# Optimization experiments

Hardware: AMD Instinct MI355X
Metric: run time of the kernel (lower is better)

The kernel has to match this reference:

```python
import jax, jax.numpy as jnp
import numpy as np

DIM = 768
HEADS = 12
HEAD_DIM = DIM // HEADS
HIDDEN = int(DIM * 1.0)  # mlp_ratio = 1.0
EPS = 1e-5


def layer_norm(x, g, b):
    mu = jnp.mean(x, axis=-1, keepdims=True)
    var = jnp.mean(jnp.square(x - mu), axis=-1, keepdims=True)
    return (x - mu) * jax.lax.rsqrt(var + EPS) * g + b


def setup_inputs() -> dict:
    key = jax.random.key(0)
    ks = jax.random.split(key, 8)
    s = 0.02
    return {
        "x": jax.random.normal(ks[0], (8, 1024, DIM), dtype=jnp.float32),
        "mask": jnp.ones((8, 1024), dtype=jnp.int32),
        "g1": jnp.ones((DIM,), jnp.float32),
        "b1": jnp.zeros((DIM,), jnp.float32),
        "w_qkv": jax.random.normal(ks[1], (DIM, 3 * DIM), jnp.float32) * s,
        "w_proj": jax.random.normal(ks[2], (DIM, DIM), jnp.float32) * s,
        "b_proj": jnp.zeros((DIM,), jnp.float32),
        "g2": jnp.ones((DIM,), jnp.float32),
        "b2": jnp.zeros((DIM,), jnp.float32),
        "w_fc1": jax.random.normal(ks[3], (DIM, HIDDEN), jnp.float32) * s,
        "b_fc1": jnp.zeros((HIDDEN,), jnp.float32),
        "w_fc2": jax.random.normal(ks[4], (HIDDEN, DIM), jnp.float32) * s,
        "b_fc2": jnp.zeros((DIM,), jnp.float32),
    }


def reference(x, mask, g1, b1, w_qkv, w_proj, b_proj, g2, b2, w_fc1, b_fc1, w_fc2, b_fc2):
    B, N, C = x.shape
    scale = HEAD_DIM ** -0.5

    # --- attention (pre-norm) ---
    h = layer_norm(x, g1, b1)
    qkv = (h @ w_qkv).reshape(B, N, 3, HEADS, HEAD_DIM)
    qkv = jnp.transpose(qkv, (2, 0, 3, 1, 4))  # 3, b, h, n, d
    q, k, v = qkv[0], qkv[1], qkv[2]

    attn = jnp.einsum("bhnd,bhmd->bhnm", q, k) * scale
    # mask: (B, N) -> pairwise mask (B, 1, N, N)
    pair = (mask[:, None, :, None] * mask[:, None, None, :]) != 0
    attn = jnp.where(pair, attn, jnp.float32(-1e9))
    attn = jax.nn.softmax(attn, axis=-1)

    o = jnp.einsum("bhnm,bhmd->bhnd", attn, v)
    o = jnp.transpose(o, (0, 2, 1, 3)).reshape(B, N, C)
    o = o @ w_proj + b_proj
    x = x + o

    # --- MLP (pre-norm) ---
    h2 = layer_norm(x, g2, b2)
    h2 = jax.nn.gelu(h2 @ w_fc1 + b_fc1, approximate=False)
    h2 = h2 @ w_fc2 + b_fc2
    return x + h2
```

## Files before the change

### kernel.cpp

```cpp
#include <hip/hip_runtime.h>
#include <stdint.h>
#include <math.h>

using short8 = __attribute__((ext_vector_type(8))) short;
using f32x4  = __attribute__((ext_vector_type(4))) float;

#define DEV __device__ __forceinline__
#define S_VMCNT(n) asm volatile("s_waitcnt vmcnt(" #n ")" ::: "memory")
#define S_LGKM(n)  asm volatile("s_waitcnt lgkmcnt(" #n ")" ::: "memory")
#define S_LGKM0()  asm volatile("s_waitcnt lgkmcnt(0)" ::: "memory")
#define SCHED0()   __builtin_amdgcn_sched_barrier(0)
#define SBAR()     __builtin_amdgcn_s_barrier()

DEV unsigned short f2bf(float f) {
    union { float f; unsigned u; } c; c.f = f;
    unsigned u = c.u;
    unsigned r = (u + 0x7FFFu + ((u >> 16) & 1u)) >> 16;
    return (unsigned short)r;
}

DEV float bf2f(unsigned short h) {
    union { unsigned u; float f; } c; c.u = ((unsigned)h) << 16;
    return c.f;
}

DEV void gld16(const unsigned short* g, unsigned short* l) {
    __builtin_amdgcn_global_load_lds(
        (const __attribute__((address_space(1))) void*)g,
        (__attribute__((address_space(3))) void*)l, 16, 0, 0);
}

DEV unsigned ldsaddr(unsigned short* p) {
    return (unsigned)(uintptr_t)(__attribute__((address_space(3))) unsigned short*)p;
}

DEV unsigned cvtpk(float lo, float hi) {
    unsigned r;
    asm("v_cvt_pk_bf16_f32 %0, %1, %2" : "=v"(r) : "v"(lo), "v"(hi));
    return r;
}

DEV uint2 tr16(unsigned addr) {
    uint2 r;
    asm volatile("ds_read_b64_tr_b16 %0, %1" : "=v"(r) : "v"(addr));
    return r;
}

__global__ __launch_bounds__(256) void k_prep(
    const float* __restrict__ x, const float* __restrict__ g,
    const float* __restrict__ b, unsigned short* __restrict__ h_out,
    unsigned short* __restrict__ xb,
    const float* __restrict__ w0, const float* __restrict__ w1,
    const float* __restrict__ w2, const float* __restrict__ w3,
    unsigned short* __restrict__ o0, unsigned short* __restrict__ o1,
    unsigned short* __restrict__ o2, unsigned short* __restrict__ o3)
{
    __shared__ float tile[32][33];
    __shared__ float red[8];
    int bid = blockIdx.x;
    int tid = threadIdx.x;

    if (bid < 8192) {
        int row = bid;
        const float* xr = x + (size_t)row * 768;
        float v0 = xr[tid], v1 = xr[tid + 256], v2 = xr[tid + 512];
        float s1 = v0 + v1 + v2;
        float s2 = v0 * v0 + v1 * v1 + v2 * v2;
#pragma unroll
        for (int off = 32; off >= 1; off >>= 1) {
            s1 += __shfl_down(s1, off);
            s2 += __shfl_down(s2, off);
        }
        int wid = tid >> 6, lane = tid & 63;
        if (lane == 0) { red[wid] = s1; red[4 + wid] = s2; }
        __syncthreads();
        s1 = red[0] + red[1] + red[2] + red[3];
        s2 = red[4] + red[5] + red[6] + red[7];
        float mu = s1 * (1.0f / 768.0f);
        float var = s2 * (1.0f / 768.0f) - mu * mu;
        float rs = rsqrtf(var + 1e-5f);
        unsigned short* orow = h_out + (size_t)row * 768;
        unsigned short* xrow = xb + (size_t)row * 768;
        orow[tid]       = f2bf((v0 - mu) * rs * g[tid]       + b[tid]);
        orow[tid + 256] = f2bf((v1 - mu) * rs * g[tid + 256] + b[tid + 256]);
        orow[tid + 512] = f2bf((v2 - mu) * rs * g[tid + 512] + b[tid + 512]);
        xrow[tid]       = f2bf(v0);
        xrow[tid + 256] = f2bf(v1);
        xrow[tid + 512] = f2bf(v2);
    } else {
        int idx = bid - 8192;
        const float* W; unsigned short* Wt; int N, n0, k0;
        if (idx < 1728) {
            W = w0; Wt = o0; N = 2304;
            n0 = (idx % 72) * 32; k0 = (idx / 72) * 32;
        } else {
            idx -= 1728;
            int z = idx / 576, r = idx % 576;
            W = (z == 0) ? w1 : (z == 1) ? w2 : w3;
            Wt = (z == 0) ? o1 : (z == 1) ? o2 : o3;
            N = 768;
            n0 = (r % 24) * 32; k0 = (r / 24) * 32;
        }
        int tx = tid & 31, ty = tid >> 5;
#pragma unroll
        for (int i = 0; i < 4; i++) {
            int k = k0 + ty + i * 8;
            tile[ty + i * 8][tx] = W[(size_t)k * N + n0 + tx];
        }
        __syncthreads();
#pragma unroll
        for (int i = 0; i < 4; i++) {
            int n = n0 + ty + i * 8;
            Wt[(size_t)n * 768 + k0 + tx] = f2bf(tile[tx][ty + i * 8]);
        }
    }
}

__global__ __launch_bounds__(256) void k_layernorm_bf(
    const unsigned short* __restrict__ xin, const float* __restrict__ g,
    const float* __restrict__ b, unsigned short* __restrict__ out)
{
    int row = blockIdx.x;
    int tid = threadIdx.x;
    const unsigned short* xr = xin + (size_t)row * 768;
    float v0 = bf2f(xr[tid]), v1 = bf2f(xr[tid + 256]), v2 = bf2f(xr[tid + 512]);
    float s1 = v0 + v1 + v2;
    float s2 = v0 * v0 + v1 * v1 + v2 * v2;
#pragma unroll
    for (int off = 32; off >= 1; off >>= 1) {
        s1 += __shfl_down(s1, off);
        s2 += __shfl_down(s2, off);
    }
    __shared__ float red[8];
    int wid = tid >> 6, lane = tid & 63;
    if (lane == 0) { red[wid] = s1; red[4 + wid] = s2; }
    __syncthreads();
    s1 = red[0] + red[1] + red[2] + red[3];
    s2 = red[4] + red[5] + red[6] + red[7];
    float mu = s1 * (1.0f / 768.0f);
    float var = s2 * (1.0f / 768.0f) - mu * mu;
    float rs = rsqrtf(var + 1e-5f);
    unsigned short* orow = out + (size_t)row * 768;
    orow[tid]       = f2bf((v0 - mu) * rs * g[tid]       + b[tid]);
    orow[tid + 256] = f2bf((v1 - mu) * rs * g[tid + 256] + b[tid + 256]);
    orow[tid + 512] = f2bf((v2 - mu) * rs * g[tid + 512] + b[tid + 512]);
}

template<int EPI, int BN>
__global__ __launch_bounds__(BN == 128 ? 512 : 256) void k_gemm(
    const unsigned short* __restrict__ A, const unsigned short* __restrict__ Bt,
    const float* __restrict__ bias, const unsigned short* __restrict__ residH,
    float* __restrict__ outF, unsigned short* __restrict__ outH,
    unsigned short* __restrict__ qb, unsigned short* __restrict__ kb,
    unsigned short* __restrict__ vtb)
{
    constexpr int KK = 768, NK = 12;
    constexpr int MI = 2;
    constexpr int NJ = 4;
    __shared__ __align__(16) unsigned short As[2][128 * 64];
    __shared__ __align__(16) unsigned short Bs[2][BN * 64];

    int tid = threadIdx.x;
    int lane = tid & 63, wid = tid >> 6;

    int gy = gridDim.y;
    int nwg = 64 * gy;
    int bid = blockIdx.x + blockIdx.y * 64;
    int nid = (bid & 7) * (nwg >> 3) + (bid >> 3);
    int bx = nid / gy;
    int by = nid - bx * gy;
    int m0 = bx * 128, n0 = by * BN;

    int wr = (BN == 128) ? (wid >> 1) * 32 : wid * 32;
    int wc = (BN == 128) ? (wid & 1) * 64 : 0;
    int fr = lane & 15, fg = lane >> 4;
    int fr7 = fr & 7;

    f32x4 zero4 = {0.f, 0.f, 0.f, 0.f};
    f32x4 acc[MI][NJ];
#pragma unroll
    for (int mi = 0; mi < MI; mi++)
#pragma unroll
        for (int nj = 0; nj < NJ; nj++) acc[mi][nj] = zero4;

    int srow = tid >> 3;
    int schk = (tid & 7) ^ ((tid >> 3) & 7);
    const unsigned short* ga = A  + (size_t)(m0 + srow) * KK + schk * 8;
    const unsigned short* gb = Bt + (size_t)(n0 + srow) * KK + schk * 8;

    auto stage = [&](int kt, int s) {
        int ko = kt * 64;
        if constexpr (BN == 128) {
            gld16(ga + ko, As[s] + wid * 512);
            gld16(ga + (size_t)64 * KK + ko, As[s] + 4096 + wid * 512);
            gld16(gb + ko, Bs[s] + wid * 512);
            gld16(gb + (size_t)64 * KK + ko, Bs[s] + 4096 + wid * 512);
        } else {
#pragma unroll
            for (int i = 0; i < 4; i++)
                gld16(ga + (size_t)i * 32 * KK + ko, As[s] + i * 2048 + wid * 512);
#pragma unroll
            for (int i = 0; i < 2; i++)
                gld16(gb + (size_t)i * 32 * KK + ko, Bs[s] + i * 2048 + wid * 512);
        }
    };

    int aoff0 = (wr + fr) * 64;
    int boff0 = (wc + fr) * 64;

    stage(0, 0);

    for (int k = 0; k < NK; ++k) {
        if (k + 1 < NK) {
            stage(k + 1, (k + 1) & 1);
            if constexpr (BN == 128) { S_VMCNT(4); } else { S_VMCNT(6); }
        } else {
            S_VMCNT(0);
        }
        SCHED0(); SBAR(); SCHED0();

        const unsigned short* Ac = As[k & 1];
        const unsigned short* Bc = Bs[k & 1];
#pragma unroll
        for (int kk = 0; kk < 2; ++kk) {
            int off = (((kk << 2) | fg) ^ fr7) * 8;
            short8 af[MI], bfv[NJ];
#pragma unroll
            for (int mi = 0; mi < MI; mi++)
                af[mi] = *(const short8*)(Ac + aoff0 + mi * 1024 + off);
#pragma unroll
            for (int nj = 0; nj < NJ; nj++)
                bfv[nj] = *(const short8*)(Bc + boff0 + nj * 1024 + off);
#pragma unroll
            for (int mi = 0; mi < MI; mi++)
#pragma unroll
                for (int nj = 0; nj < NJ; nj++)
                    acc[mi][nj] = __builtin_amdgcn_mfma_f32_16x16x32_bf16(
                        af[mi], bfv[nj], acc[mi][nj], 0, 0, 0);
        }
        SCHED0(); SBAR(); SCHED0();
    }

    if (EPI == 0 && n0 >= 1536) {
        unsigned short* Ct = &As[0][0];
#pragma unroll
        for (int mi = 0; mi < MI; mi++) {
#pragma unroll
            for (int nj = 0; nj < NJ; nj++) {
                int row = wc + nj * 16 + fr;
                int colb = wr + mi * 16 + fg * 4;
                int ch = (colb >> 3) ^ (row & 15);
                uint2 w;
                w.x = cvtpk(acc[mi][nj][0], acc[mi][nj][1]);
                w.y = cvtpk(acc[mi][nj][2], acc[mi][nj][3]);
                *(uint2*)(Ct + row * 128 + ch * 8 + (colb & 7)) = w;
            }
        }
        __syncthreads();
        int r = tid >> 2;
        int h0 = (n0 - 1536) >> 6;
        int bb = m0 >> 10;
        int nbase = m0 & 1023;
        size_t vbase = ((size_t)(bb * 12 + h0 + (r >> 6)) << 16)
                     + (size_t)(r & 63) * 1024 + nbase;
#pragma unroll
        for (int j = 0; j < 4; j++) {
            int c = (tid & 3) * 4 + j;
            int ch = c ^ (r & 15);
            uint4 v4 = *(const uint4*)(Ct + r * 128 + ch * 8);
            *(uint4*)(vtb + vbase + c * 8) = v4;
        }
        return;
    }

#pragma unroll
    for (int mi = 0; mi < MI; mi++) {
#pragma unroll
        for (int nj = 0; nj < NJ; nj++) {
#pragma unroll
            for (int i = 0; i < 4; i++) {
                int grow = m0 + wr + mi * 16 + fg * 4 + i;
                int gcol = n0 + wc + nj * 16 + fr;
                float v = acc[mi][nj][i];
                if (EPI == 0) {
                    int part = gcol / 768;
                    int wi = gcol - part * 768;
                    int head = wi >> 6, d = wi & 63;
                    int bb = grow >> 10, n = grow & 1023;
                    size_t base = ((size_t)(bb * 12 + head)) << 16;
                    unsigned short bv = f2bf(v);
                    if (part == 0) qb[base + (size_t)n * 64 + d] = bv;
                    else           kb[base + (size_t)n * 64 + d] = bv;
                } else if (EPI == 1) {
                    size_t idx = (size_t)grow * 768 + gcol;
                    outH[idx] = f2bf(v + bias[gcol] + bf2f(residH[idx]));
                } else if (EPI == 2) {
                    float t = v + bias[gcol];
                    outH[(size_t)grow * 768 + gcol] =
                        f2bf(0.5f * t * (1.0f + erff(t * 0.70710678118f)));
                } else {
                    size_t idx = (size_t)grow * 768 + gcol;
                    outF[idx] = v + bias[gcol] + bf2f(residH[idx]);
                }
            }
        }
    }
}

__global__ __launch_bounds__(512) void k_attn(
    const unsigned short* __restrict__ Q, const unsigned short* __restrict__ Kk,
    const unsigned short* __restrict__ Vt, const int* __restrict__ mask,
    unsigned short* __restrict__ O)
{
    __shared__ __align__(16) unsigned short KsA[3 * 4096];
    __shared__ __align__(16) unsigned short VsA[3 * 4096];
    __shared__ __align__(16) unsigned short PT[8 * 1024];
    __shared__ float mskf[1024];

    int tid = threadIdx.x, lane = tid & 63, wid = tid >> 6;
    int bid = blockIdx.x + blockIdx.y * 8;
    int nid = (bid & 7) * 96 + (bid >> 3);
    int qt = nid & 7;
    int bh = nid >> 3;
    int b = bh / 12;
    int hh = bh - b * 12;
    int fr = lane & 15, fg = lane >> 4;

    const unsigned short* qg = Q  + ((size_t)bh << 16);
    const unsigned short* kg = Kk + ((size_t)bh << 16);
    const unsigned short* vg = Vt + ((size_t)bh << 16);

    for (int i = tid; i < 1024; i += 512)
        mskf[i] = mask[b * 1024 + i] ? 1.f : 0.f;

    short8 qf[2];
    {
        const unsigned short* qp = qg + (size_t)(qt * 128 + wid * 16 + fr) * 64 + fg * 8;
        qf[0] = *(const short8*)(qp);
        qf[1] = *(const short8*)(qp + 32);
    }

    int srow = wid * 8 + (lane >> 3);
    int schk = (lane & 7) ^ ((lane >> 3) & 7);
    const unsigned short* kgp = kg + (size_t)srow * 64 + schk * 8;
    const unsigned short* vgp = vg + (size_t)srow * 1024 + schk * 8;

    auto stage = [&](int kn, int s) {
        gld16(kgp + (size_t)(kn * 64) * 64, &KsA[s * 4096] + wid * 512);
        gld16(vgp + kn * 64, &VsA[s * 4096] + wid * 512);
    };

    stage(0, 0);
    __syncthreads();

    f32x4 zero4 = {0.f, 0.f, 0.f, 0.f};
    f32x4 oacc[4];
    f32x4 lacc = zero4;
#pragma unroll
    for (int df = 0; df < 4; df++) oacc[df] = zero4;

    short8 ones8;
#pragma unroll
    for (int j = 0; j < 8; j++) ones8[j] = (short)0x3F80;

    const float SC = 0.125f * 1.44269504f;

    unsigned short* pw = &PT[wid * 1024];
    unsigned trbase = ldsaddr(pw) + fg * 256 + fr * 2;

    int pos0 = fg ^ (fr & 7);
    int pos1 = (fg + 4) ^ (fr & 7);

#pragma unroll
    for (int kc = 0; kc < 16; ++kc) {
        S_VMCNT(0);
        SCHED0(); SBAR(); SCHED0();
        if (kc < 15) { stage(kc + 1, (kc + 1) % 3); SCHED0(); }

        const unsigned short* Kc = &KsA[(kc % 3) * 4096];
        short8 kb0[4], kb1[4];
#pragma unroll
        for (int nf = 0; nf < 4; ++nf) {
            int row = nf * 16 + fr;
            kb0[nf] = *(const short8*)(Kc + row * 64 + pos0 * 8);
            kb1[nf] = *(const short8*)(Kc + row * 64 + pos1 * 8);
        }
        SCHED0();

        f32x4 s[4];
        if (kc > 0) {
            S_LGKM(8);
            uint2 r00 = tr16(trbase);
            uint2 r01 = tr16(trbase + 128);
            uint2 r10 = tr16(trbase + 1024);
            uint2 r11 = tr16(trbase + 1024 + 128);
            S_LGKM(4);
            SCHED0();
            __builtin_amdgcn_s_setprio(1);
#pragma unroll
            for (int nf = 0; nf < 4; ++nf) {
                f32x4 a = zero4;
                a = __builtin_amdgcn_mfma_f32_16x16x32_bf16(qf[0], kb0[nf], a, 0, 0, 0);
                a = __builtin_amdgcn_mfma_f32_16x16x32_bf16(qf[1], kb1[nf], a, 0, 0, 0);
                s[nf] = a;
            }
            __builtin_amdgcn_s_setprio(0);

            const unsigned short* Vp = &VsA[(((kc - 1) % 3)) * 4096];
            short8 vb0[4], vb1[4];
#pragma unroll
            for (int df = 0; df < 4; ++df) {
                int rv = df * 16 + fr;
                vb0[df] = *(const short8*)(Vp + rv * 64 + pos0 * 8);
                vb1[df] = *(const short8*)(Vp + rv * 64 + pos1 * 8);
            }

            union { unsigned u[4]; short8 s8; } pa0, pa1;
            pa0.u[0] = r00.x; pa0.u[1] = r00.y; pa0.u[2] = r01.x; pa0.u[3] = r01.y;
            pa1.u[0] = r10.x; pa1.u[1] = r10.y; pa1.u[2] = r11.x; pa1.u[3] = r11.y;

            uint2 w[4];
#pragma unroll
            for (int nf = 0; nf < 4; nf++) {
                float mk = mskf[kc * 64 + nf * 16 + fr];
                float p0 = __builtin_amdgcn_exp2f(s[nf][0] * SC) * mk;
                float p1 = __builtin_amdgcn_exp2f(s[nf][1] * SC) * mk;
                float p2 = __builtin_amdgcn_exp2f(s[nf][2] * SC) * mk;
                float p3 = __builtin_amdgcn_exp2f(s[nf][3] * SC) * mk;
                w[nf].x = cvtpk(p0, p1); w[nf].y = cvtpk(p2, p3);
            }

            S_LGKM0();
            SCHED0();
            __builtin_amdgcn_s_setprio(1);
#pragma unroll
            for (int df = 0; df < 4; df++) {
                oacc[df] = __builtin_amdgcn_mfma_f32_16x16x32_bf16(pa0.s8, vb0[df], oacc[df], 0, 0, 0);
                oacc[df] = __builtin_amdgcn_mfma_f32_16x16x32_bf16(pa1.s8, vb1[df], oacc[df], 0, 0, 0);
            }
            lacc = __builtin_amdgcn_mfma_f32_16x16x32_bf16(pa0.s8, ones8, lacc, 0, 0, 0);
            lacc = __builtin_amdgcn_mfma_f32_16x16x32_bf16(pa1.s8, ones8, lacc, 0, 0, 0);
            __builtin_amdgcn_s_setprio(0);

#pragma unroll
            for (int nf = 0; nf < 4; nf++)
                *(uint2*)(pw + (nf * 16 + fr) * 16 + fg * 4) = w[nf];
        } else {
            S_LGKM0();
            SCHED0();
            __builtin_amdgcn_s_setprio(1);
#pragma unroll
            for (int nf = 0; nf < 4; ++nf) {
                f32x4 a = zero4;
                a = __builtin_amdgcn_mfma_f32_16x16x32_bf16(qf[0], kb0[nf], a, 0, 0, 0);
                a = __builtin_amdgcn_mfma_f32_16x16x32_bf16(qf[1], kb1[nf], a, 0, 0, 0);
                s[nf] = a;
            }
            __builtin_amdgcn_s_setprio(0);
#pragma unroll
            for (int nf = 0; nf < 4; nf++) {
                float mk = mskf[nf * 16 + fr];
                float p0 = __builtin_amdgcn_exp2f(s[nf][0] * SC) * mk;
                float p1 = __builtin_amdgcn_exp2f(s[nf][1] * SC) * mk;
                float p2 = __builtin_amdgcn_exp2f(s[nf][2] * SC) * mk;
                float p3 = __builtin_amdgcn_exp2f(s[nf][3] * SC) * mk;
                uint2 w0; w0.x = cvtpk(p0, p1); w0.y = cvtpk(p2, p3);
                *(uint2*)(pw + (nf * 16 + fr) * 16 + fg * 4) = w0;
            }
        }
    }

    {
        uint2 r00 = tr16(trbase);
        uint2 r01 = tr16(trbase + 128);
        uint2 r10 = tr16(trbase + 1024);
        uint2 r11 = tr16(trbase + 1024 + 128);
        const unsigned short* Vp = &VsA[0];
        short8 vb0[4], vb1[4];
#pragma unroll
        for (int df = 0; df < 4; ++df) {
            int rv = df * 16 + fr;
            vb0[df] = *(const short8*)(Vp + rv * 64 + pos0 * 8);
            vb1[df] = *(const short8*)(Vp + rv * 64 + pos1 * 8);
        }
        S_LGKM0(); SCHED0();
        union { unsigned u[4]; short8 s8; } pa0, pa1;
        pa0.u[0] = r00.x; pa0.u[1] = r00.y; pa0.u[2] = r01.x; pa0.u[3] = r01.y;
        pa1.u[0] = r10.x; pa1.u[1] = r10.y; pa1.u[2] = r11.x; pa1.u[3] = r11.y;
#pragma unroll
        for (int df = 0; df < 4; df++) {
            oacc[df] = __builtin_amdgcn_mfma_f32_16x16x32_bf16(pa0.s8, vb0[df], oacc[df], 0, 0, 0);
            oacc[df] = __builtin_amdgcn_mfma_f32_16x16x32_bf16(pa1.s8, vb1[df], oacc[df], 0, 0, 0);
        }
        lacc = __builtin_amdgcn_mfma_f32_16x16x32_bf16(pa0.s8, ones8, lacc, 0, 0, 0);
        lacc = __builtin_amdgcn_mfma_f32_16x16x32_bf16(pa1.s8, ones8, lacc, 0, 0, 0);
    }

#pragma unroll
    for (int i = 0; i < 4; i++) {
        float inv = 1.0f / fmaxf(lacc[i], 1e-30f);
        size_t rowbase = ((size_t)(b * 1024 + qt * 128 + wid * 16 + fg * 4 + i)) * 768
                         + hh * 64 + fr;
#pragma unroll
        for (int df = 0; df < 4; df++)
            O[rowbase + df * 16] = f2bf(oacc[df][i] * inv);
    }
}

extern "C" void kernel_launch(void* const* d_in, const int* in_sizes, int n_in,
                              void* d_out, int out_size, void* d_ws, size_t ws_size,
                              hipStream_t stream)
{
    const float* x      = (const float*)d_in[0];
    const int*   mask   = (const int*)d_in[1];
    const float* g1     = (const float*)d_in[2];
    const float* b1     = (const float*)d_in[3];
    const float* w_qkv  = (const float*)d_in[4];
    const float* w_proj = (const float*)d_in[5];
    const float* b_proj = (const float*)d_in[6];
    const float* g2     = (const float*)d_in[7];
    const float* b2     = (const float*)d_in[8];
    const float* w_fc1  = (const float*)d_in[9];
    const float* b_fc1  = (const float*)d_in[10];
    const float* w_fc2  = (const float*)d_in[11];
    const float* b_fc2  = (const float*)d_in[12];
    float* out = (float*)d_out;

    char* ws = (char*)d_ws;
    unsigned short* wqkv_t  = (unsigned short*)(ws + 0);
    unsigned short* wproj_t = (unsigned short*)(ws + 3538944);
    unsigned short* wfc1_t  = (unsigned short*)(ws + 4718592);
    unsigned short* wfc2_t  = (unsigned short*)(ws + 5898240);
    unsigned short* bufA    = (unsigned short*)(ws + 7077888);
    unsigned short* bufB    = (unsigned short*)(ws + 19660800);
    unsigned short* qb      = (unsigned short*)(ws + 32243712);
    unsigned short* kb      = (unsigned short*)(ws + 44826624);
    unsigned short* vtb     = (unsigned short*)(ws + 57409536);
    unsigned short* x1b     = (unsigned short*)(ws + 69992448);
    unsigned short* xb      = (unsigned short*)(ws + 82575360);

    k_prep<<<8192 + 3456, 256, 0, stream>>>(x, g1, b1, bufA, xb,
        w_qkv, w_proj, w_fc1, w_fc2, wqkv_t, wproj_t, wfc1_t, wfc2_t);

    k_gemm<0, 128><<<dim3(64, 18), 512, 0, stream>>>(bufA, wqkv_t,
        nullptr, nullptr, nullptr, nullptr, qb, kb, vtb);

    k_attn<<<dim3(8, 96), 512, 0, stream>>>(qb, kb, vtb, mask, bufB);

    k_gemm<1, 64><<<dim3(64, 12), 256, 0, stream>>>(bufB, wproj_t,
        b_proj, xb, nullptr, x1b, nullptr, nullptr, nullptr);

    k_layernorm_bf<<<8192, 256, 0, stream>>>(x1b, g2, b2, bufA);

    k_gemm<2, 64><<<dim3(64, 12), 256, 0, stream>>>(bufA, wfc1_t,
        b_fc1, nullptr, nullptr, bufB, nullptr, nullptr, nullptr);

    k_gemm<3, 64><<<dim3(64, 12), 256, 0, stream>>>(bufB, wfc2_t,
        b_fc2, x1b, out, nullptr, nullptr, nullptr, nullptr);
}
```

Baseline: 158.9 us.

## Load V fragments directly from global into registers, double-buffer K in LDS

The attention kernel stops staging V tiles through shared memory. Each wave now loads its V MFMA fragments straight from global memory one step ahead, and K staging drops from a triple to a double buffer. The aim is to cut LDS traffic and footprint and remove a shared-memory round trip for V. The cost is that all eight waves of a block redundantly fetch the same V tile through the cache, with strided 16-byte loads whose latency must be hidden by the new vmcnt waits.

```diff
diff --git a/kernel.cpp b/kernel.cpp
--- a/kernel.cpp
+++ b/kernel.cpp
@@ -312,8 +312,7 @@
     const unsigned short* __restrict__ Vt, const int* __restrict__ mask,
     unsigned short* __restrict__ O)
 {
-    __shared__ __align__(16) unsigned short KsA[3 * 4096];
-    __shared__ __align__(16) unsigned short VsA[3 * 4096];
+    __shared__ __align__(16) unsigned short KsA[2 * 4096];
     __shared__ __align__(16) unsigned short PT[8 * 1024];
     __shared__ float mskf[1024];
 
@@ -340,17 +339,17 @@
         qf[1] = *(const short8*)(qp + 32);
     }
 
-    int srow = wid * 8 + (lane >> 3);
-    int schk = (lane & 7) ^ ((lane >> 3) & 7);
+    int srow = tid >> 3;
+    int schk = (tid & 7) ^ ((tid >> 3) & 7);
     const unsigned short* kgp = kg + (size_t)srow * 64 + schk * 8;
-    const unsigned short* vgp = vg + (size_t)srow * 1024 + schk * 8;
-
-    auto stage = [&](int kn, int s) {
+
+    auto stageK = [&](int kn, int s) {
         gld16(kgp + (size_t)(kn * 64) * 64, &KsA[s * 4096] + wid * 512);
-        gld16(vgp + kn * 64, &VsA[s * 4096] + wid * 512);
     };
 
-    stage(0, 0);
+    const unsigned short* vbase = vg + (size_t)fr * 1024 + fg * 8;
+
+    stageK(0, 0);
     __syncthreads();
 
     f32x4 zero4 = {0.f, 0.f, 0.f, 0.f};
@@ -375,9 +374,20 @@
     for (int kc = 0; kc < 16; ++kc) {
         S_VMCNT(0);
         SCHED0(); SBAR(); SCHED0();
-        if (kc < 15) { stage(kc + 1, (kc + 1) % 3); SCHED0(); }
-
-        const unsigned short* Kc = &KsA[(kc % 3) * 4096];
+
+        short8 vb0[4], vb1[4];
+        if (kc > 0) {
+            const unsigned short* vc = vbase + (kc - 1) * 64;
+#pragma unroll
+            for (int df = 0; df < 4; ++df) {
+                vb0[df] = *(const short8*)(vc + (size_t)df * 16384);
+                vb1[df] = *(const short8*)(vc + (size_t)df * 16384 + 32);
+            }
+            SCHED0();
+        }
+        if (kc < 15) { stageK(kc + 1, (kc + 1) & 1); SCHED0(); }
+
+        const unsigned short* Kc = &KsA[(kc & 1) * 4096];
         short8 kb0[4], kb1[4];
 #pragma unroll
         for (int nf = 0; nf < 4; ++nf) {
@@ -406,15 +416,6 @@
             }
             __builtin_amdgcn_s_setprio(0);
 
-            const unsigned short* Vp = &VsA[(((kc - 1) % 3)) * 4096];
-            short8 vb0[4], vb1[4];
-#pragma unroll
-            for (int df = 0; df < 4; ++df) {
-                int rv = df * 16 + fr;
-                vb0[df] = *(const short8*)(Vp + rv * 64 + pos0 * 8);
-                vb1[df] = *(const short8*)(Vp + rv * 64 + pos1 * 8);
-            }
-
             union { unsigned u[4]; short8 s8; } pa0, pa1;
             pa0.u[0] = r00.x; pa0.u[1] = r00.y; pa0.u[2] = r01.x; pa0.u[3] = r01.y;
             pa1.u[0] = r10.x; pa1.u[1] = r10.y; pa1.u[2] = r11.x; pa1.u[3] = r11.y;
@@ -430,6 +431,7 @@
                 w[nf].x = cvtpk(p0, p1); w[nf].y = cvtpk(p2, p3);
             }
 
+            if (kc < 15) { S_VMCNT(1); } else { S_VMCNT(0); }
             S_LGKM0();
             SCHED0();
             __builtin_amdgcn_s_setprio(1);
@@ -471,19 +473,18 @@
     }
 
     {
+        short8 vb0[4], vb1[4];
+        const unsigned short* vc = vbase + 15 * 64;
+#pragma unroll
+        for (int df = 0; df < 4; ++df) {
+            vb0[df] = *(const short8*)(vc + (size_t)df * 16384);
+            vb1[df] = *(const short8*)(vc + (size_t)df * 16384 + 32);
+        }
         uint2 r00 = tr16(trbase);
         uint2 r01 = tr16(trbase + 128);
         uint2 r10 = tr16(trbase + 1024);
         uint2 r11 = tr16(trbase + 1024 + 128);
-        const unsigned short* Vp = &VsA[0];
-        short8 vb0[4], vb1[4];
-#pragma unroll
-        for (int df = 0; df < 4; ++df) {
-            int rv = df * 16 + fr;
-            vb0[df] = *(const short8*)(Vp + rv * 64 + pos0 * 8);
-            vb1[df] = *(const short8*)(Vp + rv * 64 + pos1 * 8);
-        }
-        S_LGKM0(); SCHED0();
+        S_VMCNT(0); S_LGKM0(); SCHED0();
         union { unsigned u[4]; short8 s8; } pa0, pa1;
         pa0.u[0] = r00.x; pa0.u[1] = r00.y; pa0.u[2] = r01.x; pa0.u[3] = r01.y;
         pa1.u[0] = r10.x; pa1.u[1] = r10.y; pa1.u[2] = r11.x; pa1.u[3] = r11.y;
```

After: 237.8 us. +49.6%, slower.

## Rewrite attention with 32x32x16 MFMA and in-register P transpose via permlane32_swap

Applied to the files above, without the earlier changes.

The attention kernel moves from 16x16x32 to 32x32x16 MFMA tiles, computing S^T = K·Q so the probabilities land in a layout that v_permlane32_swap turns into the A operand for the PV product. This removes the per-warp LDS staging buffer and the ds_read_b64_tr_b16 transposes, along with the one-iteration software pipeline that deferred PV by a step. Blocks drop to 256 threads with 4 waves, each handling 32 query rows, and the staging loads are doubled per thread. The trade is fewer waves per block, less overlap between QK and PV, and more accumulator registers per wave.

```diff
diff --git a/kernel.cpp b/kernel.cpp
--- a/kernel.cpp
+++ b/kernel.cpp
@@ -4,11 +4,10 @@
 
 using short8 = __attribute__((ext_vector_type(8))) short;
 using f32x4  = __attribute__((ext_vector_type(4))) float;
+using f32x16 = __attribute__((ext_vector_type(16))) float;
 
 #define DEV __device__ __forceinline__
 #define S_VMCNT(n) asm volatile("s_waitcnt vmcnt(" #n ")" ::: "memory")
-#define S_LGKM(n)  asm volatile("s_waitcnt lgkmcnt(" #n ")" ::: "memory")
-#define S_LGKM0()  asm volatile("s_waitcnt lgkmcnt(0)" ::: "memory")
 #define SCHED0()   __builtin_amdgcn_sched_barrier(0)
 #define SBAR()     __builtin_amdgcn_s_barrier()
 
@@ -30,19 +29,9 @@
         (__attribute__((address_space(3))) void*)l, 16, 0, 0);
 }
 
-DEV unsigned ldsaddr(unsigned short* p) {
-    return (unsigned)(uintptr_t)(__attribute__((address_space(3))) unsigned short*)p;
-}
-
 DEV unsigned cvtpk(float lo, float hi) {
     unsigned r;
     asm("v_cvt_pk_bf16_f32 %0, %1, %2" : "=v"(r) : "v"(lo), "v"(hi));
-    return r;
-}
-
-DEV uint2 tr16(unsigned addr) {
-    uint2 r;
-    asm volatile("ds_read_b64_tr_b16 %0, %1" : "=v"(r) : "v"(addr));
     return r;
 }
 
@@ -307,15 +296,14 @@
     }
 }
 
-__global__ __launch_bounds__(512) void k_attn(
+__global__ __launch_bounds__(256) void k_attn(
     const unsigned short* __restrict__ Q, const unsigned short* __restrict__ Kk,
     const unsigned short* __restrict__ Vt, const int* __restrict__ mask,
     unsigned short* __restrict__ O)
 {
     __shared__ __align__(16) unsigned short KsA[3 * 4096];
     __shared__ __align__(16) unsigned short VsA[3 * 4096];
-    __shared__ __align__(16) unsigned short PT[8 * 1024];
-    __shared__ float mskf[1024];
+    __shared__ __align__(16) float mskf[1024];
 
     int tid = threadIdx.x, lane = tid & 63, wid = tid >> 6;
     int bid = blockIdx.x + blockIdx.y * 8;
@@ -324,186 +312,112 @@
     int bh = nid >> 3;
     int b = bh / 12;
     int hh = bh - b * 12;
-    int fr = lane & 15, fg = lane >> 4;
+    int c = lane & 31, h = lane >> 5;
 
     const unsigned short* qg = Q  + ((size_t)bh << 16);
     const unsigned short* kg = Kk + ((size_t)bh << 16);
     const unsigned short* vg = Vt + ((size_t)bh << 16);
 
-    for (int i = tid; i < 1024; i += 512)
+    for (int i = tid; i < 1024; i += 256)
         mskf[i] = mask[b * 1024 + i] ? 1.f : 0.f;
 
-    short8 qf[2];
+    short8 qf[4];
     {
-        const unsigned short* qp = qg + (size_t)(qt * 128 + wid * 16 + fr) * 64 + fg * 8;
-        qf[0] = *(const short8*)(qp);
-        qf[1] = *(const short8*)(qp + 32);
-    }
-
-    int srow = wid * 8 + (lane >> 3);
-    int schk = (lane & 7) ^ ((lane >> 3) & 7);
+        const unsigned short* qp = qg + (size_t)(qt * 128 + wid * 32 + c) * 64 + h * 8;
+#pragma unroll
+        for (int ks = 0; ks < 4; ks++)
+            qf[ks] = *(const short8*)(qp + ks * 16);
+    }
+
+    int srow = tid >> 3;
+    int schk = (tid & 7) ^ (srow & 7);
     const unsigned short* kgp = kg + (size_t)srow * 64 + schk * 8;
     const unsigned short* vgp = vg + (size_t)srow * 1024 + schk * 8;
 
     auto stage = [&](int kn, int s) {
-        gld16(kgp + (size_t)(kn * 64) * 64, &KsA[s * 4096] + wid * 512);
-        gld16(vgp + kn * 64, &VsA[s * 4096] + wid * 512);
+        unsigned short* Kd = &KsA[s * 4096];
+        unsigned short* Vd = &VsA[s * 4096];
+        gld16(kgp + (size_t)(kn * 64) * 64, Kd + wid * 512);
+        gld16(kgp + (size_t)(kn * 64 + 32) * 64, Kd + 2048 + wid * 512);
+        gld16(vgp + kn * 64, Vd + wid * 512);
+        gld16(vgp + 32 * 1024 + kn * 64, Vd + 2048 + wid * 512);
     };
 
     stage(0, 0);
     __syncthreads();
 
-    f32x4 zero4 = {0.f, 0.f, 0.f, 0.f};
-    f32x4 oacc[4];
-    f32x4 lacc = zero4;
-#pragma unroll
-    for (int df = 0; df < 4; df++) oacc[df] = zero4;
+    f32x16 oacc0, oacc1, lacc;
+#pragma unroll
+    for (int i = 0; i < 16; i++) { oacc0[i] = 0.f; oacc1[i] = 0.f; lacc[i] = 0.f; }
 
     short8 ones8;
 #pragma unroll
     for (int j = 0; j < 8; j++) ones8[j] = (short)0x3F80;
 
     const float SC = 0.125f * 1.44269504f;
-
-    unsigned short* pw = &PT[wid * 1024];
-    unsigned trbase = ldsaddr(pw) + fg * 256 + fr * 2;
-
-    int pos0 = fg ^ (fr & 7);
-    int pos1 = (fg + 4) ^ (fr & 7);
-
-#pragma unroll
+    int c7 = c & 7;
+
     for (int kc = 0; kc < 16; ++kc) {
         S_VMCNT(0);
         SCHED0(); SBAR(); SCHED0();
         if (kc < 15) { stage(kc + 1, (kc + 1) % 3); SCHED0(); }
 
         const unsigned short* Kc = &KsA[(kc % 3) * 4096];
-        short8 kb0[4], kb1[4];
-#pragma unroll
-        for (int nf = 0; nf < 4; ++nf) {
-            int row = nf * 16 + fr;
-            kb0[nf] = *(const short8*)(Kc + row * 64 + pos0 * 8);
-            kb1[nf] = *(const short8*)(Kc + row * 64 + pos1 * 8);
-        }
-        SCHED0();
-
-        f32x4 s[4];
-        if (kc > 0) {
-            S_LGKM(8);
-            uint2 r00 = tr16(trbase);
-            uint2 r01 = tr16(trbase + 128);
-            uint2 r10 = tr16(trbase + 1024);
-            uint2 r11 = tr16(trbase + 1024 + 128);
-            S_LGKM(4);
-            SCHED0();
+        const unsigned short* Vc = &VsA[(kc % 3) * 4096];
+
+        unsigned aw[2][8];
+#pragma unroll
+        for (int kf = 0; kf < 2; ++kf) {
+            f32x16 s;
+#pragma unroll
+            for (int i = 0; i < 16; i++) s[i] = 0.f;
             __builtin_amdgcn_s_setprio(1);
 #pragma unroll
-            for (int nf = 0; nf < 4; ++nf) {
-                f32x4 a = zero4;
-                a = __builtin_amdgcn_mfma_f32_16x16x32_bf16(qf[0], kb0[nf], a, 0, 0, 0);
-                a = __builtin_amdgcn_mfma_f32_16x16x32_bf16(qf[1], kb1[nf], a, 0, 0, 0);
-                s[nf] = a;
+            for (int ks = 0; ks < 4; ++ks) {
+                int row = kf * 32 + c;
+                short8 kfr = *(const short8*)(Kc + row * 64 + (((ks << 1) | h) ^ c7) * 8);
+                s = __builtin_amdgcn_mfma_f32_32x32x16_bf16(kfr, qf[ks], s, 0, 0, 0);
             }
             __builtin_amdgcn_s_setprio(0);
-
-            const unsigned short* Vp = &VsA[(((kc - 1) % 3)) * 4096];
-            short8 vb0[4], vb1[4];
-#pragma unroll
-            for (int df = 0; df < 4; ++df) {
-                int rv = df * 16 + fr;
-                vb0[df] = *(const short8*)(Vp + rv * 64 + pos0 * 8);
-                vb1[df] = *(const short8*)(Vp + rv * 64 + pos1 * 8);
+#pragma unroll
+            for (int a = 0; a < 4; ++a) {
+                float4 m4 = *(const float4*)(&mskf[kc * 64 + kf * 32 + a * 8 + h * 4]);
+                float p0 = __builtin_amdgcn_exp2f(s[a * 4 + 0] * SC) * m4.x;
+                float p1 = __builtin_amdgcn_exp2f(s[a * 4 + 1] * SC) * m4.y;
+                float p2 = __builtin_amdgcn_exp2f(s[a * 4 + 2] * SC) * m4.z;
+                float p3 = __builtin_amdgcn_exp2f(s[a * 4 + 3] * SC) * m4.w;
+                aw[kf][a * 2 + 0] = cvtpk(p0, p1);
+                aw[kf][a * 2 + 1] = cvtpk(p2, p3);
             }
-
-            union { unsigned u[4]; short8 s8; } pa0, pa1;
-            pa0.u[0] = r00.x; pa0.u[1] = r00.y; pa0.u[2] = r01.x; pa0.u[3] = r01.y;
-            pa1.u[0] = r10.x; pa1.u[1] = r10.y; pa1.u[2] = r11.x; pa1.u[3] = r11.y;
-
-            uint2 w[4];
-#pragma unroll
-            for (int nf = 0; nf < 4; nf++) {
-                float mk = mskf[kc * 64 + nf * 16 + fr];
-                float p0 = __builtin_amdgcn_exp2f(s[nf][0] * SC) * mk;
-                float p1 = __builtin_amdgcn_exp2f(s[nf][1] * SC) * mk;
-                float p2 = __builtin_amdgcn_exp2f(s[nf][2] * SC) * mk;
-                float p3 = __builtin_amdgcn_exp2f(s[nf][3] * SC) * mk;
-                w[nf].x = cvtpk(p0, p1); w[nf].y = cvtpk(p2, p3);
-            }
-
-            S_LGKM0();
-            SCHED0();
+        }
+
+#pragma unroll
+        for (int t = 0; t < 4; ++t) {
+            int kf = t >> 1, ib = (t & 1) * 4;
+            unsigned u0 = aw[kf][ib + 0], v0 = aw[kf][ib + 2];
+            unsigned u1 = aw[kf][ib + 1], v1 = aw[kf][ib + 3];
+            asm volatile("v_permlane32_swap_b32 %0, %1" : "+v"(u0), "+v"(v0));
+            asm volatile("v_permlane32_swap_b32 %0, %1" : "+v"(u1), "+v"(v1));
+            union { unsigned u[4]; short8 s8; } pa;
+            pa.u[0] = u0; pa.u[1] = u1; pa.u[2] = v0; pa.u[3] = v1;
+
+            short8 vb0 = *(const short8*)(Vc + c * 64 + (((t << 1) | h) ^ c7) * 8);
+            short8 vb1 = *(const short8*)(Vc + (32 + c) * 64 + (((t << 1) | h) ^ c7) * 8);
             __builtin_amdgcn_s_setprio(1);
-#pragma unroll
-            for (int df = 0; df < 4; df++) {
-                oacc[df] = __builtin_amdgcn_mfma_f32_16x16x32_bf16(pa0.s8, vb0[df], oacc[df], 0, 0, 0);
-                oacc[df] = __builtin_amdgcn_mfma_f32_16x16x32_bf16(pa1.s8, vb1[df], oacc[df], 0, 0, 0);
-            }
-            lacc = __builtin_amdgcn_mfma_f32_16x16x32_bf16(pa0.s8, ones8, lacc, 0, 0, 0);
-            lacc = __builtin_amdgcn_mfma_f32_16x16x32_bf16(pa1.s8, ones8, lacc, 0, 0, 0);
+            oacc0 = __builtin_amdgcn_mfma_f32_32x32x16_bf16(pa.s8, vb0, oacc0, 0, 0, 0);
+            oacc1 = __builtin_amdgcn_mfma_f32_32x32x16_bf16(pa.s8, vb1, oacc1, 0, 0, 0);
+            lacc  = __builtin_amdgcn_mfma_f32_32x32x16_bf16(pa.s8, ones8, lacc, 0, 0, 0);
             __builtin_amdgcn_s_setprio(0);
-
-#pragma unroll
-            for (int nf = 0; nf < 4; nf++)
-                *(uint2*)(pw + (nf * 16 + fr) * 16 + fg * 4) = w[nf];
-        } else {
-            S_LGKM0();
-            SCHED0();
-            __builtin_amdgcn_s_setprio(1);
-#pragma unroll
-            for (int nf = 0; nf < 4; ++nf) {
-                f32x4 a = zero4;
-                a = __builtin_amdgcn_mfma_f32_16x16x32_bf16(qf[0], kb0[nf], a, 0, 0, 0);
-                a = __builtin_amdgcn_mfma_f32_16x16x32_bf16(qf[1], kb1[nf], a, 0, 0, 0);
-                s[nf] = a;
-            }
-            __builtin_amdgcn_s_setprio(0);
-#pragma unroll
-            for (int nf = 0; nf < 4; nf++) {
-                float mk = mskf[nf * 16 + fr];
-                float p0 = __builtin_amdgcn_exp2f(s[nf][0] * SC) * mk;
-                float p1 = __builtin_amdgcn_exp2f(s[nf][1] * SC) * mk;
-                float p2 = __builtin_amdgcn_exp2f(s[nf][2] * SC) * mk;
-                float p3 = __builtin_amdgcn_exp2f(s[nf][3] * SC) * mk;
-                uint2 w0; w0.x = cvtpk(p0, p1); w0.y = cvtpk(p2, p3);
-                *(uint2*)(pw + (nf * 16 + fr) * 16 + fg * 4) = w0;
-            }
-        }
-    }
-
-    {
-        uint2 r00 = tr16(trbase);
-        uint2 r01 = tr16(trbase + 128);
-        uint2 r10 = tr16(trbase + 1024);
-        uint2 r11 = tr16(trbase + 1024 + 128);
-        const unsigned short* Vp = &VsA[0];
-        short8 vb0[4], vb1[4];
-#pragma unroll
-        for (int df = 0; df < 4; ++df) {
-            int rv = df * 16 + fr;
-            vb0[df] = *(const short8*)(Vp + rv * 64 + pos0 * 8);
-            vb1[df] = *(const short8*)(Vp + rv * 64 + pos1 * 8);
-        }
-        S_LGKM0(); SCHED0();
-        union { unsigned u[4]; short8 s8; } pa0, pa1;
-        pa0.u[0] = r00.x; pa0.u[1] = r00.y; pa0.u[2] = r01.x; pa0.u[3] = r01.y;
-        pa1.u[0] = r10.x; pa1.u[1] = r10.y; pa1.u[2] = r11.x; pa1.u[3] = r11.y;
-#pragma unroll
-        for (int df = 0; df < 4; df++) {
-            oacc[df] = __builtin_amdgcn_mfma_f32_16x16x32_bf16(pa0.s8, vb0[df], oacc[df], 0, 0, 0);
-            oacc[df] = __builtin_amdgcn_mfma_f32_16x16x32_bf16(pa1.s8, vb1[df], oacc[df], 0, 0, 0);
-        }
-        lacc = __builtin_amdgcn_mfma_f32_16x16x32_bf16(pa0.s8, ones8, lacc, 0, 0, 0);
-        lacc = __builtin_amdgcn_mfma_f32_16x16x32_bf16(pa1.s8, ones8, lacc, 0, 0, 0);
-    }
-
-#pragma unroll
-    for (int i = 0; i < 4; i++) {
-        float inv = 1.0f / fmaxf(lacc[i], 1e-30f);
-        size_t rowbase = ((size_t)(b * 1024 + qt * 128 + wid * 16 + fg * 4 + i)) * 768
-                         + hh * 64 + fr;
-#pragma unroll
-        for (int df = 0; df < 4; df++)
-            O[rowbase + df * 16] = f2bf(oacc[df][i] * inv);
+        }
+    }
+
+#pragma unroll
+    for (int reg = 0; reg < 16; ++reg) {
+        int q = (reg & 3) + 8 * (reg >> 2) + 4 * h;
+        float inv = 1.0f / fmaxf(lacc[reg], 1e-30f);
+        size_t rowbase = ((size_t)(b * 1024 + qt * 128 + wid * 32 + q)) * 768 + hh * 64 + c;
+        O[rowbase]      = f2bf(oacc0[reg] * inv);
+        O[rowbase + 32] = f2bf(oacc1[reg] * inv);
     }
 }
 
@@ -545,7 +459,7 @@
     k_gemm<0, 128><<<dim3(64, 18), 512, 0, stream>>>(bufA, wqkv_t,
         nullptr, nullptr, nullptr, nullptr, qb, kb, vtb);
 
-    k_attn<<<dim3(8, 96), 512, 0, stream>>>(qb, kb, vtb, mask, bufB);
+    k_attn<<<dim3(8, 96), 256, 0, stream>>>(qb, kb, vtb, mask, bufB);
 
     k_gemm<1, 64><<<dim3(64, 12), 256, 0, stream>>>(bufB, wproj_t,
         b_proj, xb, nullptr, x1b, nullptr, nullptr, nullptr);
```

Result: no change. 159.7 us (+0.5%).
